# Kernel tuning notes

Hardware: AMD Instinct MI355X
Metric: run time of the kernel (lower is better)

The kernel has to match this reference:

```python
import jax, jax.numpy as jnp
import numpy as np

N_PROJECT = 100000
N_COMPANY = 50000
N_EDGES = 1000000
INPUT_DIM = 256
HIDDEN_DIM = 128
NUM_LAYERS = 2
EPS = 1e-12


def setup_inputs() -> dict:
    key = jax.random.key(0)
    ks = jax.random.split(key, 10)
    return {
        "x_project": jax.random.normal(ks[0], (N_PROJECT, INPUT_DIM), jnp.float32),
        "x_company": jax.random.normal(ks[1], (N_COMPANY, INPUT_DIM), jnp.float32),
        "W_project": jax.random.normal(ks[2], (INPUT_DIM, HIDDEN_DIM), jnp.float32) * 0.05,
        "b_project": jax.random.normal(ks[3], (HIDDEN_DIM,), jnp.float32) * 0.05,
        "W_company": jax.random.normal(ks[4], (INPUT_DIM, HIDDEN_DIM), jnp.float32) * 0.05,
        "b_company": jax.random.normal(ks[5], (HIDDEN_DIM,), jnp.float32) * 0.05,
        "pc_src": jax.random.randint(ks[6], (N_EDGES,), 0, N_PROJECT, jnp.int32),
        "pc_dst": jax.random.randint(ks[7], (N_EDGES,), 0, N_COMPANY, jnp.int32),
        "cp_src": jax.random.randint(ks[8], (N_EDGES,), 0, N_COMPANY, jnp.int32),
        "cp_dst": jax.random.randint(ks[9], (N_EDGES,), 0, N_PROJECT, jnp.int32),
    }


def _rel_aggregate(x_src, row, col, num_src, num_dst):
    # D_src^-1/2 A D_dst^-1/2 normalized gather-scale-scatter_add for one relation.
    ones = jnp.ones(row.shape[0], jnp.float32)
    deg_s = jax.ops.segment_sum(ones, row, num_segments=num_src)
    deg_d = jax.ops.segment_sum(ones, col, num_segments=num_dst)
    inv_s = jnp.where(deg_s > 0, deg_s ** -0.5, 0.0)
    inv_d = jnp.where(deg_d > 0, deg_d ** -0.5, 0.0)
    w = inv_s[row] * inv_d[col]                      # [E]
    msg = x_src[row] * w[:, None]                    # [E, H]
    return jax.ops.segment_sum(msg, col, num_segments=num_dst)  # [num_dst, H]


def reference(x_project, x_company, W_project, b_project, W_company, b_company,
              pc_src, pc_dst, cp_src, cp_dst):
    h_p = x_project @ W_project + b_project          # [Np, H]
    h_c = x_company @ W_company + b_company          # [Nc, H]
    acc_p, acc_c = h_p, h_c
    for _ in range(NUM_LAYERS):
        new_p = _rel_aggregate(h_c, cp_src, cp_dst, N_COMPANY, N_PROJECT)
        new_c = _rel_aggregate(h_p, pc_src, pc_dst, N_PROJECT, N_COMPANY)
        h_p, h_c = new_p, new_c
        acc_p = acc_p + h_p
        acc_c = acc_c + h_c
    scale = 1.0 / (NUM_LAYERS + 1)
    out_p = acc_p * scale
    out_c = acc_c * scale
    # F.normalize(p=2, dim=-1)
    out_p = out_p / jnp.maximum(jnp.linalg.norm(out_p, axis=-1, keepdims=True), EPS)
    out_c = out_c / jnp.maximum(jnp.linalg.norm(out_c, axis=-1, keepdims=True), EPS)
    return out_p, out_c
```

## Files before the change

### kernel.cpp

```cpp
#include <hip/hip_runtime.h>
#include <hip/hip_bf16.h>
#include <math.h>

#define HD 128
#define KD 256
#define CAP 64
#define CAPA 96
#define BA 128

typedef __attribute__((ext_vector_type(8))) short bf16x8;
typedef __attribute__((ext_vector_type(4))) float f32x4;

__device__ __forceinline__ unsigned short bfbits(float x) {
    __hip_bfloat16 h = __float2bfloat16(x);
    return *(unsigned short*)&h;
}
__device__ __forceinline__ unsigned int pack_bf2(float a, float b) {
    __hip_bfloat162 h;
    h.x = __float2bfloat16(a);
    h.y = __float2bfloat16(b);
    return *(unsigned int*)&h;
}
__device__ __forceinline__ float2 unpack_bf2(unsigned int u) {
    __hip_bfloat162 h = *(__hip_bfloat162*)&u;
    return __bfloat1622float2(h);
}
__device__ __forceinline__ bf16x8 cvt8(float4 a, float4 b) {
    bf16x8 r;
    r[0] = (short)bfbits(a.x); r[1] = (short)bfbits(a.y);
    r[2] = (short)bfbits(a.z); r[3] = (short)bfbits(a.w);
    r[4] = (short)bfbits(b.x); r[5] = (short)bfbits(b.y);
    r[6] = (short)bfbits(b.z); r[7] = (short)bfbits(b.w);
    return r;
}

__global__ void convW2(const float* __restrict__ WA, unsigned short* __restrict__ WtA,
                       const float* __restrict__ WB, unsigned short* __restrict__ WtB) {
    int idx = blockIdx.x * 256 + threadIdx.x;
    const float* W = (idx < KD * HD) ? WA : WB;
    unsigned short* Wt = (idx < KD * HD) ? WtA : WtB;
    int id = idx & (KD * HD - 1);
    int j    = id & 7;
    int lane = (id >> 3) & 63;
    int nt   = (id >> 9) & 7;
    int kc   = id >> 12;
    int k = kc * 32 + (lane >> 4) * 8 + j;
    int c = nt * 16 + (lane & 15);
    Wt[id] = bfbits(W[k * HD + c]);
}

__device__ __forceinline__ void gemm_body(
        char* smem, const float* __restrict__ X, const unsigned short* __restrict__ Wt,
        const float* __restrict__ bias, unsigned short* __restrict__ out0,
        int M, int tile) {
    float (*eps)[16][68] = (float (*)[16][68])smem;

    const int t = threadIdx.x;
    const int lane = t & 63;
    const int w = t >> 6;
    const int lr = lane & 15;
    const int kb = lane >> 4;
    const int rbase = tile * 128;

    f32x4 acc[2][8];
    #pragma unroll
    for (int nt = 0; nt < 8; ++nt) {
        float bv = bias[nt * 16 + lr];
        acc[0][nt] = (f32x4){bv, bv, bv, bv};
        acc[1][nt] = (f32x4){bv, bv, bv, bv};
    }

    const float4* X4 = (const float4*)X;
    const int r0 = rbase + w * 32 + lr;
    const int r1 = r0 + 16;
    const size_t rr0 = (size_t)((r0 < M) ? r0 : 0) * 64 + kb * 2;
    const size_t rr1 = (size_t)((r1 < M) ? r1 : 0) * 64 + kb * 2;

    float4 xf[2][4];
    #pragma unroll
    for (int s = 0; s < 2; ++s) {
        xf[s][0] = X4[rr0 + s * 8];
        xf[s][1] = X4[rr0 + s * 8 + 1];
        xf[s][2] = X4[rr1 + s * 8];
        xf[s][3] = X4[rr1 + s * 8 + 1];
    }

    #pragma unroll
    for (int kc = 0; kc < 8; ++kc) {
        const int s = kc & 1;
        bf16x8 a0 = cvt8(xf[s][0], xf[s][1]);
        bf16x8 a1 = cvt8(xf[s][2], xf[s][3]);
        if (kc < 6) {
            xf[s][0] = X4[rr0 + (kc + 2) * 8];
            xf[s][1] = X4[rr0 + (kc + 2) * 8 + 1];
            xf[s][2] = X4[rr1 + (kc + 2) * 8];
            xf[s][3] = X4[rr1 + (kc + 2) * 8 + 1];
        }
        const unsigned short* wb = Wt + ((size_t)(kc * 8) * 64 + lane) * 8;
        #pragma unroll
        for (int nt = 0; nt < 8; ++nt) {
            bf16x8 b = *(const bf16x8*)(wb + (size_t)nt * 512);
            acc[0][nt] = __builtin_amdgcn_mfma_f32_16x16x32_bf16(a0, b, acc[0][nt], 0, 0, 0);
            acc[1][nt] = __builtin_amdgcn_mfma_f32_16x16x32_bf16(a1, b, acc[1][nt], 0, 0, 0);
        }
    }

    const int er = lane >> 2;
    const int ec = lane & 3;
    #pragma unroll
    for (int mt = 0; mt < 2; ++mt) {
        #pragma unroll
        for (int hf = 0; hf < 2; ++hf) {
            __syncthreads();
            #pragma unroll
            for (int nt = 0; nt < 4; ++nt)
                #pragma unroll
                for (int reg = 0; reg < 4; ++reg)
                    eps[w][kb * 4 + reg][nt * 16 + lr] = acc[mt][hf * 4 + nt][reg];
            __syncthreads();
            const int g = rbase + w * 32 + mt * 16 + er;
            if (g < M) {
                #pragma unroll
                for (int i = 0; i < 4; ++i) {
                    const int f4c = ec + i * 4;
                    float4 v = *(const float4*)&eps[w][er][f4c * 4];
                    uint2 u;
                    u.x = pack_bf2(v.x, v.y);
                    u.y = pack_bf2(v.z, v.w);
                    *(uint2*)(out0 + (size_t)g * HD + hf * 64 + f4c * 4) = u;
                }
            }
        }
    }
}

__launch_bounds__(256, 4)
__global__ void fusedAG(
        const int* __restrict__ cps, const int* __restrict__ cpd,
        int* __restrict__ db0, int* __restrict__ sb0, int* cntD0, int* cntS0,
        const int* __restrict__ pcs, const int* __restrict__ pcd,
        int* __restrict__ db1, int* __restrict__ sb1, int* cntD1, int* cntS1,
        int E, int G0, int G1,
        const float* Xp, const unsigned short* WtP, const float* bp,
        unsigned short* h0p, int Np, int GP,
        const float* Xc, const unsigned short* WtC, const float* bc,
        unsigned short* h0c, int Nc) {
    __shared__ __align__(16) char smem[17408];
    const int b = blockIdx.x;
    if (b < 2 * BA) {
        int* curD = (int*)smem;
        int* curS = curD + 512;
        const int rel = b >> 7;
        const int ib  = b & (BA - 1);
        const int* src = rel ? pcs : cps;
        const int* dst = rel ? pcd : cpd;
        int* db   = rel ? db1 : db0;
        int* sb   = rel ? sb1 : sb0;
        int* cntD = rel ? cntD1 : cntD0;
        int* cntS = rel ? cntS1 : cntS0;
        const int GD  = rel ? G1 : G0;
        const int GS  = rel ? G0 : G1;

        for (int i = threadIdx.x; i < 512; i += 256) { curD[i] = 0; curS[i] = 0; }
        __syncthreads();

        const int chunk = (E + BA - 1) / BA;
        const int e0 = ib * chunk;
        const int e1 = (e0 + chunk < E) ? e0 + chunk : E;
        for (int e = e0 + (int)threadIdx.x; e < e1; e += 256) {
            const int s = src[e];
            const int d = dst[e];
            const int gd = d >> 8;
            const int pd = atomicAdd(&curD[gd], 1);
            if (pd < CAPA)
                db[((size_t)(ib * GD + gd)) * CAPA + pd] = ((d & 255) << 17) | s;
            const int gs = s >> 8;
            const int ps = atomicAdd(&curS[gs], 1);
            if (ps < CAPA)
                sb[((size_t)(ib * GS + gs)) * CAPA + ps] = s;
        }
        __syncthreads();
        for (int g = threadIdx.x; g < GD; g += 256)
            cntD[ib * GD + g] = (curD[g] < CAPA) ? curD[g] : CAPA;
        for (int g = threadIdx.x; g < GS; g += 256)
            cntS[ib * GS + g] = (curS[g] < CAPA) ? curS[g] : CAPA;
        return;
    }
    const int gFlat = b - 2 * BA;
    if (gFlat < GP)
        gemm_body(smem, Xp, WtP, bp, h0p, Np, gFlat);
    else
        gemm_body(smem, Xc, WtC, bc, h0c, Nc, gFlat - GP);
}

__launch_bounds__(256)
__global__ void csrbuild(
        const int* __restrict__ db0, const int* cntD0, int* csr0, int* degs0,
        const int* __restrict__ db1, const int* cntD1, int* csr1, int* degs1,
        const int* __restrict__ sb0, const int* cntS0, int* hist0,
        const int* __restrict__ sb1, const int* cntS1, int* hist1,
        int G0, int G1, int Np, int Nc) {
    __shared__ int rows[256 * 64];
    const int r = blockIdx.x;
    int g, GD, M; const int *bkt, *cnt; int *outp, *degs; bool isCSR;
    if (r < G0) {
        g = r; GD = G0; M = Np; bkt = db0; cnt = cntD0;
        outp = csr0; degs = degs0; isCSR = true;
    } else if (r < G0 + G1) {
        g = r - G0; GD = G1; M = Nc; bkt = db1; cnt = cntD1;
        outp = csr1; degs = degs1; isCSR = true;
    } else if (r < G0 + 2 * G1) {
        g = r - G0 - G1; GD = G1; M = Nc; bkt = sb0; cnt = cntS0;
        outp = hist0; degs = hist0; isCSR = false;
    } else {
        g = r - G0 - 2 * G1; GD = G0; M = Np; bkt = sb1; cnt = cntS1;
        outp = hist1; degs = hist1; isCSR = false;
    }
    const int base = g << 8;
    const int rowsN = ((M - base) < 256) ? (M - base) : 256;
    const int total = BA * CAPA;

    if (isCSR) {
        for (int i = threadIdx.x; i < 256; i += 256) rows[(i << 6) + 63] = 0;
        __syncthreads();
        for (int idx = threadIdx.x; idx < total; idx += 256) {
            const int bb = idx / CAPA;
            const int i  = idx - bb * CAPA;
            if (i < cnt[bb * GD + g]) {
                const unsigned int v =
                    (unsigned int)bkt[((size_t)(bb * GD + g)) * CAPA + i];
                const int dloc = (int)(v >> 17);
                const int s = (int)(v & 0x1FFFF);
                const int p = atomicAdd(&rows[(dloc << 6) + 63], 1);
                if (p < 63) rows[(dloc << 6) + p] = s;
            }
        }
        __syncthreads();
        uint4* dst4 = (uint4*)(outp + ((size_t)base << 6));
        const uint4* src4 = (const uint4*)rows;
        for (int q = threadIdx.x; q < rowsN * 16; q += 256) dst4[q] = src4[q];
        for (int i = threadIdx.x; i < rowsN; i += 256) {
            const int c = rows[(i << 6) + 63];
            degs[base + i] = (c < 63) ? c : 63;
        }
    } else {
        for (int i = threadIdx.x; i < 256; i += 256) rows[i] = 0;
        __syncthreads();
        for (int idx = threadIdx.x; idx < total; idx += 256) {
            const int bb = idx / CAPA;
            const int i  = idx - bb * CAPA;
            if (i < cnt[bb * GD + g]) {
                const int s = bkt[((size_t)(bb * GD + g)) * CAPA + i];
                atomicAdd(&rows[s - base], 1);
            }
        }
        __syncthreads();
        for (int i = threadIdx.x; i < rowsN; i += 256) degs[base + i] = rows[i];
    }
}

__device__ __forceinline__ void agg_gather(const int* __restrict__ degs,
                                           const int* __restrict__ ssrc,
                                           const int* __restrict__ scnt,
                                           const unsigned short* __restrict__ hsrc,
                                           int row, int lane, int q, int cl,
                                           float4& accA, float4& accB) {
    const int deg = degs[row];
    accA = make_float4(0.f, 0.f, 0.f, 0.f);
    accB = make_float4(0.f, 0.f, 0.f, 0.f);
    if (deg > 0) {
        const float id = rsqrtf((float)deg);
        const int n = (deg < CAP) ? deg : CAP;
        int sl = 0; float wl = 0.f;
        if (lane < n) {
            sl = ssrc[((size_t)row << 6) + lane];
            wl = rsqrtf((float)scnt[sl]);
        }
        for (int jj = 0; jj < n; jj += 4) {
            const int j = jj + q;
            const int s = __shfl(sl, j);
            const float wt = __shfl(wl, j) * id;
            const uint4 u = *(const uint4*)(hsrc + (size_t)s * HD + cl * 8);
            const float2 f0 = unpack_bf2(u.x);
            const float2 f1 = unpack_bf2(u.y);
            const float2 f2 = unpack_bf2(u.z);
            const float2 f3 = unpack_bf2(u.w);
            accA.x = fmaf(f0.x, wt, accA.x);
            accA.y = fmaf(f0.y, wt, accA.y);
            accA.z = fmaf(f1.x, wt, accA.z);
            accA.w = fmaf(f1.y, wt, accA.w);
            accB.x = fmaf(f2.x, wt, accB.x);
            accB.y = fmaf(f2.y, wt, accB.y);
            accB.z = fmaf(f3.x, wt, accB.z);
            accB.w = fmaf(f3.y, wt, accB.w);
        }
    }
    accA.x += __shfl_xor(accA.x, 16); accA.y += __shfl_xor(accA.y, 16);
    accA.z += __shfl_xor(accA.z, 16); accA.w += __shfl_xor(accA.w, 16);
    accB.x += __shfl_xor(accB.x, 16); accB.y += __shfl_xor(accB.y, 16);
    accB.z += __shfl_xor(accB.z, 16); accB.w += __shfl_xor(accB.w, 16);
    accA.x += __shfl_xor(accA.x, 32); accA.y += __shfl_xor(accA.y, 32);
    accA.z += __shfl_xor(accA.z, 32); accA.w += __shfl_xor(accA.w, 32);
    accB.x += __shfl_xor(accB.x, 32); accB.y += __shfl_xor(accB.y, 32);
    accB.z += __shfl_xor(accB.z, 32); accB.w += __shfl_xor(accB.w, 32);
}

__global__ void agg_dual(const int* degsA, const int* ssrcA, const int* scntA,
                         const unsigned short* hsrcA, unsigned short* hdstA, int MA,
                         const int* degsB, const int* ssrcB, const int* scntB,
                         const unsigned short* hsrcB, unsigned short* hdstB, int MB) {
    const int bA = (MA + 3) / 4;
    const int lane = threadIdx.x & 63;
    const int q  = lane >> 4;
    const int cl = lane & 15;
    int row;
    const int *degs, *ssrc, *scnt;
    const unsigned short* hsrc; unsigned short* hdst; int M;
    if ((int)blockIdx.x < bA) {
        row = blockIdx.x * 4 + (threadIdx.x >> 6);
        degs = degsA; ssrc = ssrcA; scnt = scntA; hsrc = hsrcA; hdst = hdstA; M = MA;
    } else {
        row = (blockIdx.x - bA) * 4 + (threadIdx.x >> 6);
        degs = degsB; ssrc = ssrcB; scnt = scntB; hsrc = hsrcB; hdst = hdstB; M = MB;
    }
    if (row >= M) return;
    float4 accA, accB;
    agg_gather(degs, ssrc, scnt, hsrc, row, lane, q, cl, accA, accB);
    if (q == 0) {
        uint4 u;
        u.x = pack_bf2(accA.x, accA.y);
        u.y = pack_bf2(accA.z, accA.w);
        u.z = pack_bf2(accB.x, accB.y);
        u.w = pack_bf2(accB.z, accB.w);
        *(uint4*)(hdst + (size_t)row * HD + cl * 8) = u;
    }
}

__global__ void agg_norm_dual(const int* degsA, const int* ssrcA, const int* scntA,
                              const unsigned short* hsrcA, const unsigned short* h0A,
                              const unsigned short* h1A, float* outA, int MA,
                              const int* degsB, const int* ssrcB, const int* scntB,
                              const unsigned short* hsrcB, const unsigned short* h0B,
                              const unsigned short* h1B, float* outB, int MB) {
    const int bA = (MA + 3) / 4;
    const int lane = threadIdx.x & 63;
    const int q  = lane >> 4;
    const int cl = lane & 15;
    int row;
    const int *degs, *ssrc, *scnt;
    const unsigned short *hsrc, *h0, *h1; float* outp; int M;
    if ((int)blockIdx.x < bA) {
        row = blockIdx.x * 4 + (threadIdx.x >> 6);
        degs = degsA; ssrc = ssrcA; scnt = scntA; hsrc = hsrcA;
        h0 = h0A; h1 = h1A; outp = outA; M = MA;
    } else {
        row = (blockIdx.x - bA) * 4 + (threadIdx.x >> 6);
        degs = degsB; ssrc = ssrcB; scnt = scntB; hsrc = hsrcB;
        h0 = h0B; h1 = h1B; outp = outB; M = MB;
    }
    if (row >= M) return;
    float4 accA, accB;
    agg_gather(degs, ssrc, scnt, hsrc, row, lane, q, cl, accA, accB);

    float2 h2;
    if (q == 0)      h2 = make_float2(accA.x, accA.y);
    else if (q == 1) h2 = make_float2(accA.z, accA.w);
    else if (q == 2) h2 = make_float2(accB.x, accB.y);
    else             h2 = make_float2(accB.z, accB.w);

    const int c = cl * 8 + q * 2;
    const size_t base = (size_t)row * HD + c;
    float2 h0v = unpack_bf2(*(const unsigned int*)(h0 + base));
    float2 h1v = unpack_bf2(*(const unsigned int*)(h1 + base));
    const float sc = 1.0f / 3.0f;
    float vx = (h0v.x + h1v.x + h2.x) * sc;
    float vy = (h0v.y + h1v.y + h2.y) * sc;
    float ss = vx * vx + vy * vy;
    #pragma unroll
    for (int off = 1; off < 64; off <<= 1) ss += __shfl_xor(ss, off);
    float inv = 1.0f / fmaxf(sqrtf(ss), 1e-12f);
    *(float2*)(outp + base) = make_float2(vx * inv, vy * inv);
}

extern "C" void kernel_launch(void* const* d_in, const int* in_sizes, int n_in,
                              void* d_out, int out_size, void* d_ws, size_t ws_size,
                              hipStream_t stream) {
    const float* x_p = (const float*)d_in[0];
    const float* x_c = (const float*)d_in[1];
    const float* W_p = (const float*)d_in[2];
    const float* b_p = (const float*)d_in[3];
    const float* W_c = (const float*)d_in[4];
    const float* b_c = (const float*)d_in[5];
    const int* pcs = (const int*)d_in[6];
    const int* pcd = (const int*)d_in[7];
    const int* cps = (const int*)d_in[8];
    const int* cpd = (const int*)d_in[9];

    const int Np = in_sizes[0] / KD;
    const int Nc = in_sizes[1] / KD;
    const int E  = in_sizes[6];

    const int G0 = (Np + 255) >> 8;
    const int G1 = (Nc + 255) >> 8;

    int* scp = (int*)d_ws;
    int* spc = scp + ((size_t)Np << 6);
    int* c_cps = spc + ((size_t)Nc << 6);
    int* c_pcs = c_cps + Nc;
    int* c_cpd = c_pcs + Np;
    int* c_pcd = c_cpd + Np;
    unsigned short* bufP0 = (unsigned short*)(c_pcd + Nc);
    unsigned short* bufC0 = bufP0 + (size_t)Np * HD;
    unsigned short* WtP = bufC0 + (size_t)Nc * HD;
    unsigned short* WtC = WtP + KD * HD;
    int* db0 = (int*)(WtC + KD * HD);
    int* db1 = db0 + (size_t)BA * G0 * CAPA;
    int* sb0 = db1 + (size_t)BA * G1 * CAPA;
    int* sb1 = sb0 + (size_t)BA * G1 * CAPA;
    int* cntD0 = sb1 + (size_t)BA * G0 * CAPA;
    int* cntD1 = cntD0 + BA * G0;
    int* cntS0 = cntD1 + BA * G1;
    int* cntS1 = cntS0 + BA * G1;
    unsigned short* bufP1 = (unsigned short*)db0;
    unsigned short* bufC1 = bufP1 + (size_t)Np * HD;

    float* outP = (float*)d_out;
    float* outC = outP + (size_t)Np * HD;

    const int GP = (Np + 127) / 128;
    const int GC = (Nc + 127) / 128;

    convW2<<<(2 * KD * HD) / 256, 256, 0, stream>>>(W_p, WtP, W_c, WtC);

    fusedAG<<<2 * BA + GP + GC, 256, 0, stream>>>(
        cps, cpd, db0, sb0, cntD0, cntS0,
        pcs, pcd, db1, sb1, cntD1, cntS1,
        E, G0, G1,
        x_p, WtP, b_p, bufP0, Np, GP,
        x_c, WtC, b_c, bufC0, Nc);

    csrbuild<<<2 * (G0 + G1), 256, 0, stream>>>(
        db0, cntD0, scp, c_cpd,
        db1, cntD1, spc, c_pcd,
        sb0, cntS0, c_cps,
        sb1, cntS1, c_pcs,
        G0, G1, Np, Nc);

    const int bP = (Np + 3) / 4, bC = (Nc + 3) / 4;

    agg_dual<<<bP + bC, 256, 0, stream>>>(
        c_cpd, scp, c_cps, bufC0, bufP1, Np,
        c_pcd, spc, c_pcs, bufP0, bufC1, Nc);

    agg_norm_dual<<<bP + bC, 256, 0, stream>>>(
        c_cpd, scp, c_cps, bufC1, bufP0, bufP1, outP, Np,
        c_pcd, spc, c_pcs, bufP1, bufC0, bufC1, outC, Nc);
}
```

Before: 380.8 us.

## Split GEMM from edge bucketing and stage bf16 weights in LDS

The edge-bucketing pass now shares a kernel with the weight conversion, and the projection GEMM becomes two separate launches, one per node type. Each GEMM block stages the bf16 weights in LDS in two halves instead of reading them from global memory per MFMA, and the epilogue writes all 128 columns in one pass. The aim is to cut global weight traffic and epilogue barriers. The cost is one extra launch, lost overlap between bucketing and GEMM, more LDS per block and lower occupancy (launch bounds 3).

Result: faster. 368.9 us (-3.1%).

```diff
diff --git a/kernel.cpp b/kernel.cpp
--- a/kernel.cpp
+++ b/kernel.cpp
@@ -34,33 +34,79 @@
     return r;
 }
 
-__global__ void convW2(const float* __restrict__ WA, unsigned short* __restrict__ WtA,
-                       const float* __restrict__ WB, unsigned short* __restrict__ WtB) {
-    int idx = blockIdx.x * 256 + threadIdx.x;
-    const float* W = (idx < KD * HD) ? WA : WB;
-    unsigned short* Wt = (idx < KD * HD) ? WtA : WtB;
-    int id = idx & (KD * HD - 1);
-    int j    = id & 7;
-    int lane = (id >> 3) & 63;
-    int nt   = (id >> 9) & 7;
-    int kc   = id >> 12;
-    int k = kc * 32 + (lane >> 4) * 8 + j;
-    int c = nt * 16 + (lane & 15);
-    Wt[id] = bfbits(W[k * HD + c]);
-}
-
-__device__ __forceinline__ void gemm_body(
-        char* smem, const float* __restrict__ X, const unsigned short* __restrict__ Wt,
-        const float* __restrict__ bias, unsigned short* __restrict__ out0,
-        int M, int tile) {
-    float (*eps)[16][68] = (float (*)[16][68])smem;
+__launch_bounds__(256)
+__global__ void phaseA(
+        const int* __restrict__ cps, const int* __restrict__ cpd,
+        int* __restrict__ db0, int* __restrict__ sb0, int* cntD0, int* cntS0,
+        const int* __restrict__ pcs, const int* __restrict__ pcd,
+        int* __restrict__ db1, int* __restrict__ sb1, int* cntD1, int* cntS1,
+        int E, int G0, int G1,
+        const float* __restrict__ WA, unsigned short* __restrict__ WtA,
+        const float* __restrict__ WB, unsigned short* __restrict__ WtB) {
+    __shared__ int curD[512], curS[512];
+    const int b = blockIdx.x;
+    if (b >= 2 * BA) {
+        int idx = (b - 2 * BA) * 256 + threadIdx.x;
+        const float* W = (idx < KD * HD) ? WA : WB;
+        unsigned short* Wt = (idx < KD * HD) ? WtA : WtB;
+        int id = idx & (KD * HD - 1);
+        int j = id & 7, lane = (id >> 3) & 63, nt = (id >> 9) & 7, kc = id >> 12;
+        int k = kc * 32 + (lane >> 4) * 8 + j;
+        int c = nt * 16 + (lane & 15);
+        Wt[id] = bfbits(W[k * HD + c]);
+        return;
+    }
+    const int rel = b >> 7;
+    const int ib  = b & (BA - 1);
+    const int* src = rel ? pcs : cps;
+    const int* dst = rel ? pcd : cpd;
+    int* db   = rel ? db1 : db0;
+    int* sb   = rel ? sb1 : sb0;
+    int* cntD = rel ? cntD1 : cntD0;
+    int* cntS = rel ? cntS1 : cntS0;
+    const int GD  = rel ? G1 : G0;
+    const int GS  = rel ? G0 : G1;
+
+    for (int i = threadIdx.x; i < 512; i += 256) { curD[i] = 0; curS[i] = 0; }
+    __syncthreads();
+
+    const int chunk = (E + BA - 1) / BA;
+    const int e0 = ib * chunk;
+    const int e1 = (e0 + chunk < E) ? e0 + chunk : E;
+    for (int e = e0 + (int)threadIdx.x; e < e1; e += 256) {
+        const int s = src[e];
+        const int d = dst[e];
+        const int gd = d >> 8;
+        const int pd = atomicAdd(&curD[gd], 1);
+        if (pd < CAPA)
+            db[((size_t)(ib * GD + gd)) * CAPA + pd] = ((d & 255) << 17) | s;
+        const int gs = s >> 8;
+        const int ps = atomicAdd(&curS[gs], 1);
+        if (ps < CAPA)
+            sb[((size_t)(ib * GS + gs)) * CAPA + ps] = s;
+    }
+    __syncthreads();
+    for (int g = threadIdx.x; g < GD; g += 256)
+        cntD[ib * GD + g] = (curD[g] < CAPA) ? curD[g] : CAPA;
+    for (int g = threadIdx.x; g < GS; g += 256)
+        cntS[ib * GS + g] = (curS[g] < CAPA) ? curS[g] : CAPA;
+}
+
+__launch_bounds__(256, 3)
+__global__ void gemm_mfma(const float* __restrict__ X, const unsigned short* __restrict__ Wt,
+                          const float* __restrict__ bias,
+                          unsigned short* __restrict__ out0, int M) {
+    __shared__ __align__(16) char smem[34816];
+    uint4* lds4 = (uint4*)smem;
+    const unsigned short* lsh = (const unsigned short*)smem;
+    float (*eps)[16][132] = (float (*)[16][132])smem;
 
     const int t = threadIdx.x;
     const int lane = t & 63;
     const int w = t >> 6;
     const int lr = lane & 15;
     const int kb = lane >> 4;
-    const int rbase = tile * 128;
+    const int rbase = blockIdx.x * 128;
 
     f32x4 acc[2][8];
     #pragma unroll
@@ -71,6 +117,7 @@
     }
 
     const float4* X4 = (const float4*)X;
+    const uint4* Wg4 = (const uint4*)Wt;
     const int r0 = rbase + w * 32 + lr;
     const int r1 = r0 + 16;
     const size_t rr0 = (size_t)((r0 < M) ? r0 : 0) * 64 + kb * 2;
@@ -86,7 +133,17 @@
     }
 
     #pragma unroll
+    for (int i = 0; i < 8; ++i) { int q = t + i * 256; lds4[q] = Wg4[q]; }
+    __syncthreads();
+
+    #pragma unroll
     for (int kc = 0; kc < 8; ++kc) {
+        if (kc == 4) {
+            __syncthreads();
+            #pragma unroll
+            for (int i = 0; i < 8; ++i) { int q = t + i * 256; lds4[q] = Wg4[2048 + q]; }
+            __syncthreads();
+        }
         const int s = kc & 1;
         bf16x8 a0 = cvt8(xf[s][0], xf[s][1]);
         bf16x8 a1 = cvt8(xf[s][2], xf[s][3]);
@@ -96,101 +153,40 @@
             xf[s][2] = X4[rr1 + (kc + 2) * 8];
             xf[s][3] = X4[rr1 + (kc + 2) * 8 + 1];
         }
-        const unsigned short* wb = Wt + ((size_t)(kc * 8) * 64 + lane) * 8;
+        const int slot = kc & 3;
         #pragma unroll
         for (int nt = 0; nt < 8; ++nt) {
-            bf16x8 b = *(const bf16x8*)(wb + (size_t)nt * 512);
+            bf16x8 b = *(const bf16x8*)&lsh[(((slot * 8 + nt) * 64) + lane) * 8];
             acc[0][nt] = __builtin_amdgcn_mfma_f32_16x16x32_bf16(a0, b, acc[0][nt], 0, 0, 0);
             acc[1][nt] = __builtin_amdgcn_mfma_f32_16x16x32_bf16(a1, b, acc[1][nt], 0, 0, 0);
         }
     }
+    __syncthreads();
 
     const int er = lane >> 2;
     const int ec = lane & 3;
     #pragma unroll
     for (int mt = 0; mt < 2; ++mt) {
         #pragma unroll
-        for (int hf = 0; hf < 2; ++hf) {
-            __syncthreads();
+        for (int nt = 0; nt < 8; ++nt)
             #pragma unroll
-            for (int nt = 0; nt < 4; ++nt)
-                #pragma unroll
-                for (int reg = 0; reg < 4; ++reg)
-                    eps[w][kb * 4 + reg][nt * 16 + lr] = acc[mt][hf * 4 + nt][reg];
-            __syncthreads();
-            const int g = rbase + w * 32 + mt * 16 + er;
-            if (g < M) {
-                #pragma unroll
-                for (int i = 0; i < 4; ++i) {
-                    const int f4c = ec + i * 4;
-                    float4 v = *(const float4*)&eps[w][er][f4c * 4];
-                    uint2 u;
-                    u.x = pack_bf2(v.x, v.y);
-                    u.y = pack_bf2(v.z, v.w);
-                    *(uint2*)(out0 + (size_t)g * HD + hf * 64 + f4c * 4) = u;
-                }
+            for (int reg = 0; reg < 4; ++reg)
+                eps[w][kb * 4 + reg][nt * 16 + lr] = acc[mt][nt][reg];
+        __syncthreads();
+        const int g = rbase + w * 32 + mt * 16 + er;
+        if (g < M) {
+            #pragma unroll
+            for (int i = 0; i < 8; ++i) {
+                const int f4c = ec + i * 4;
+                float4 v = *(const float4*)&eps[w][er][f4c * 4];
+                uint2 u;
+                u.x = pack_bf2(v.x, v.y);
+                u.y = pack_bf2(v.z, v.w);
+                *(uint2*)(out0 + (size_t)g * HD + f4c * 4) = u;
             }
         }
-    }
-}
-
-__launch_bounds__(256, 4)
-__global__ void fusedAG(
-        const int* __restrict__ cps, const int* __restrict__ cpd,
-        int* __restrict__ db0, int* __restrict__ sb0, int* cntD0, int* cntS0,
-        const int* __restrict__ pcs, const int* __restrict__ pcd,
-        int* __restrict__ db1, int* __restrict__ sb1, int* cntD1, int* cntS1,
-        int E, int G0, int G1,
-        const float* Xp, const unsigned short* WtP, const float* bp,
-        unsigned short* h0p, int Np, int GP,
-        const float* Xc, const unsigned short* WtC, const float* bc,
-        unsigned short* h0c, int Nc) {
-    __shared__ __align__(16) char smem[17408];
-    const int b = blockIdx.x;
-    if (b < 2 * BA) {
-        int* curD = (int*)smem;
-        int* curS = curD + 512;
-        const int rel = b >> 7;
-        const int ib  = b & (BA - 1);
-        const int* src = rel ? pcs : cps;
-        const int* dst = rel ? pcd : cpd;
-        int* db   = rel ? db1 : db0;
-        int* sb   = rel ? sb1 : sb0;
-        int* cntD = rel ? cntD1 : cntD0;
-        int* cntS = rel ? cntS1 : cntS0;
-        const int GD  = rel ? G1 : G0;
-        const int GS  = rel ? G0 : G1;
-
-        for (int i = threadIdx.x; i < 512; i += 256) { curD[i] = 0; curS[i] = 0; }
-        __syncthreads();
-
-        const int chunk = (E + BA - 1) / BA;
-        const int e0 = ib * chunk;
-        const int e1 = (e0 + chunk < E) ? e0 + chunk : E;
-        for (int e = e0 + (int)threadIdx.x; e < e1; e += 256) {
-            const int s = src[e];
-            const int d = dst[e];
-            const int gd = d >> 8;
-            const int pd = atomicAdd(&curD[gd], 1);
-            if (pd < CAPA)
-                db[((size_t)(ib * GD + gd)) * CAPA + pd] = ((d & 255) << 17) | s;
-            const int gs = s >> 8;
-            const int ps = atomicAdd(&curS[gs], 1);
-            if (ps < CAPA)
-                sb[((size_t)(ib * GS + gs)) * CAPA + ps] = s;
-        }
-        __syncthreads();
-        for (int g = threadIdx.x; g < GD; g += 256)
-            cntD[ib * GD + g] = (curD[g] < CAPA) ? curD[g] : CAPA;
-        for (int g = threadIdx.x; g < GS; g += 256)
-            cntS[ib * GS + g] = (curS[g] < CAPA) ? curS[g] : CAPA;
-        return;
-    }
-    const int gFlat = b - 2 * BA;
-    if (gFlat < GP)
-        gemm_body(smem, Xp, WtP, bp, h0p, Np, gFlat);
-    else
-        gemm_body(smem, Xc, WtC, bc, h0c, Nc, gFlat - GP);
+        __syncthreads();
+    }
 }
 
 __launch_bounds__(256)
@@ -430,14 +426,13 @@
     const int GP = (Np + 127) / 128;
     const int GC = (Nc + 127) / 128;
 
-    convW2<<<(2 * KD * HD) / 256, 256, 0, stream>>>(W_p, WtP, W_c, WtC);
-
-    fusedAG<<<2 * BA + GP + GC, 256, 0, stream>>>(
+    phaseA<<<2 * BA + 256, 256, 0, stream>>>(
         cps, cpd, db0, sb0, cntD0, cntS0,
         pcs, pcd, db1, sb1, cntD1, cntS1,
-        E, G0, G1,
-        x_p, WtP, b_p, bufP0, Np, GP,
-        x_c, WtC, b_c, bufC0, Nc);
+        E, G0, G1, W_p, WtP, W_c, WtC);
+
+    gemm_mfma<<<GP, 256, 0, stream>>>(x_p, WtP, b_p, bufP0, Np);
+    gemm_mfma<<<GC, 256, 0, stream>>>(x_c, WtC, b_c, bufC0, Nc);
 
     csrbuild<<<2 * (G0 + G1), 256, 0, stream>>>(
         db0, cntD0, scp, c_cpd,
```
